# Kernel optimization log

Measured on AMD Instinct MI355X. Metric: run time of the kernel, lower is better.

## Reference

```python
import jax, jax.numpy as jnp
import numpy as np

B, N, H, HD = 2, 512, 1024, 512


def setup_inputs() -> dict:
    key = jax.random.key(0)
    ks = jax.random.split(key, 9)
    s = 0.02
    return {
        "emb": jax.random.normal(ks[0], (B, N, H), jnp.float32),
        # start detector: Linear(H->HD), ReLU, Linear(HD->1)
        "W_s1": jax.random.normal(ks[1], (H, HD), jnp.float32) * s,
        "b_s1": jax.random.normal(ks[2], (HD,), jnp.float32) * s,
        "w_s2": jax.random.normal(ks[3], (HD,), jnp.float32) * s,
        "b_s2": jax.random.normal(ks[4], (), jnp.float32) * s,
        # end detector: Linear(2H->HD), ReLU, Linear(HD->1)
        "W_e1": jax.random.normal(ks[5], (2 * H, HD), jnp.float32) * s,
        "b_e1": jax.random.normal(ks[6], (HD,), jnp.float32) * s,
        "w_e2": jax.random.normal(ks[7], (HD,), jnp.float32) * s,
        "b_e2": jax.random.normal(ks[8], (), jnp.float32) * s,
    }


def reference(emb, W_s1, b_s1, w_s2, b_s2, W_e1, b_e1, w_e2, b_e2):
    # start logits: (B, N)
    h_s = jax.nn.relu(jnp.einsum("bnh,hd->bnd", emb, W_s1) + b_s1)
    start_logits = jnp.einsum("bnd,d->bn", h_s, w_s2) + b_s2

    # end logits: math of cat([start_rep, end_rep]) @ W_e1 done as split matmuls
    # (avoids materializing the (B,N,N,2H) concat buffer)
    W1_start, W1_end = W_e1[:H], W_e1[H:]
    a = jnp.einsum("bih,hd->bid", emb, W1_start)  # (B, N, HD) start-token part
    c = jnp.einsum("bjh,hd->bjd", emb, W1_end)    # (B, N, HD) end-token part
    h_e = jax.nn.relu(a[:, :, None, :] + c[:, None, :, :] + b_e1)  # (B, N, N, HD)
    end_logits = jnp.einsum("bijd,d->bij", h_e, w_e2) + b_e2       # (B, N, N)

    return (start_logits, end_logits)
```

## Files before the change

kernel.cpp:

```cpp
#include <hip/hip_runtime.h>
#include <hip/hip_bf16.h>


typedef float f32x4 __attribute__((ext_vector_type(4)));
typedef float f32x2 __attribute__((ext_vector_type(2)));
typedef __bf16 bf16x8 __attribute__((ext_vector_type(8)));

static __device__ __forceinline__ unsigned short f2bf(float f) {
  unsigned int u = __builtin_bit_cast(unsigned int, f);
  u += 0x7FFFu + ((u >> 16) & 1u);
  return (unsigned short)(u >> 16);
}

__global__ __launch_bounds__(256) void prep(
    const float* __restrict__ emb, const float* __restrict__ W_s1,
    const float* __restrict__ W_e1, const float* __restrict__ b_s2,
    unsigned short* __restrict__ emb_bf, unsigned short* __restrict__ Wt_s,
    unsigned short* __restrict__ Wt_e, float* __restrict__ out) {
  __shared__ float tile[32][33];
  int bx = blockIdx.x, t = threadIdx.x;
  if (bx < 512) {
    int i = bx * 2048 + t * 8;
    f32x4 v0 = *(const f32x4*)&emb[i];
    f32x4 v1 = *(const f32x4*)&emb[i + 4];
    ushort4 o0, o1;
    o0.x = f2bf(v0[0]); o0.y = f2bf(v0[1]);
    o0.z = f2bf(v0[2]); o0.w = f2bf(v0[3]);
    o1.x = f2bf(v1[0]); o1.y = f2bf(v1[1]);
    o1.z = f2bf(v1[2]); o1.w = f2bf(v1[3]);
    *(ushort4*)&emb_bf[i] = o0;
    *(ushort4*)&emb_bf[i + 4] = o1;
  } else if (bx < 2048) {
    const float* in;
    unsigned short* o;
    int R, tid;
    if (bx < 1024) { tid = bx - 512;  in = W_s1; o = Wt_s; R = 1024; }
    else           { tid = bx - 1024; in = W_e1; o = Wt_e; R = 2048; }
    int r0 = (tid >> 4) * 32, c0 = (tid & 15) * 32;
    int a = t >> 3, b4 = t & 7;
    f32x4 v = *(const f32x4*)&in[(size_t)(r0 + a) * 512 + c0 + b4 * 4];
    tile[a][b4 * 4 + 0] = v[0];
    tile[a][b4 * 4 + 1] = v[1];
    tile[a][b4 * 4 + 2] = v[2];
    tile[a][b4 * 4 + 3] = v[3];
    __syncthreads();
    ushort4 o4;
    o4.x = f2bf(tile[b4 * 4 + 0][a]);
    o4.y = f2bf(tile[b4 * 4 + 1][a]);
    o4.z = f2bf(tile[b4 * 4 + 2][a]);
    o4.w = f2bf(tile[b4 * 4 + 3][a]);
    *(ushort4*)&o[(size_t)(c0 + a) * R + r0 + b4 * 4] = o4;
  } else {
    float v = b_s2[0];
    f32x4 o = {v, v, v, v};
    *(f32x4*)&out[t * 4] = o;
  }
}

__global__ __launch_bounds__(128) void gemm_fused(
    const unsigned short* __restrict__ Aemb,
    const unsigned short* __restrict__ Wt_s,
    const unsigned short* __restrict__ Wt_e,
    const float* __restrict__ b_s1, const float* __restrict__ w_s2,
    const float* __restrict__ b_e1, float* __restrict__ out,
    float* __restrict__ A_mat, unsigned short* __restrict__ C_bf) {
  __shared__ unsigned short Al[64][72];
  __shared__ unsigned short Bl[32][72];
  int z = blockIdx.z;
  int n0 = blockIdx.x * 32;
  int m0 = blockIdx.y * 64;
  const unsigned short* Bmat = (z == 0) ? Wt_s : Wt_e;
  int bstride = (z == 0) ? 1024 : 2048;
  int bofs = (z == 2) ? 1024 : 0;

  int t = threadIdx.x, lane = t & 63, wave = t >> 6;
  int wm = wave * 32;
  int lm = lane & 15, g = lane >> 4;

  f32x4 acc[2][2];
#pragma unroll
  for (int mi = 0; mi < 2; ++mi)
#pragma unroll
    for (int ni = 0; ni < 2; ++ni) acc[mi][ni] = (f32x4){0.f, 0.f, 0.f, 0.f};

  int ar = t >> 1, ah = (t & 1) * 32;
  int br = t >> 2, bs = (t & 3) * 16;
  for (int k0 = 0; k0 < 1024; k0 += 64) {
    __syncthreads();
    const unsigned short* ap = &Aemb[(size_t)(m0 + ar) * 1024 + k0 + ah];
    *(uint4*)&Al[ar][ah + 0]  = *(const uint4*)(ap + 0);
    *(uint4*)&Al[ar][ah + 8]  = *(const uint4*)(ap + 8);
    *(uint4*)&Al[ar][ah + 16] = *(const uint4*)(ap + 16);
    *(uint4*)&Al[ar][ah + 24] = *(const uint4*)(ap + 24);
    const unsigned short* bp =
        &Bmat[(size_t)(n0 + br) * bstride + bofs + k0 + bs];
    *(uint4*)&Bl[br][bs + 0] = *(const uint4*)(bp + 0);
    *(uint4*)&Bl[br][bs + 8] = *(const uint4*)(bp + 8);
    __syncthreads();
#pragma unroll
    for (int kk = 0; kk < 2; ++kk) {
      bf16x8 af[2], bf[2];
#pragma unroll
      for (int mi = 0; mi < 2; ++mi)
        af[mi] = *(const bf16x8*)&Al[wm + mi * 16 + lm][kk * 32 + g * 8];
#pragma unroll
      for (int ni = 0; ni < 2; ++ni)
        bf[ni] = *(const bf16x8*)&Bl[ni * 16 + lm][kk * 32 + g * 8];
#pragma unroll
      for (int mi = 0; mi < 2; ++mi)
#pragma unroll
        for (int ni = 0; ni < 2; ++ni)
          acc[mi][ni] = __builtin_amdgcn_mfma_f32_16x16x32_bf16(
              af[mi], bf[ni], acc[mi][ni], 0, 0, 0);
    }
  }

  int col0 = n0 + lm, col1 = n0 + 16 + lm;
  if (z == 0) {
    float bs0 = b_s1[col0], bs1 = b_s1[col1];
    float ws0 = w_s2[col0], ws1 = w_s2[col1];
#pragma unroll
    for (int mi = 0; mi < 2; ++mi)
#pragma unroll
      for (int r = 0; r < 4; ++r) {
        float s = fmaxf(acc[mi][0][r] + bs0, 0.f) * ws0 +
                  fmaxf(acc[mi][1][r] + bs1, 0.f) * ws1;
        s += __shfl_xor(s, 1);
        s += __shfl_xor(s, 2);
        s += __shfl_xor(s, 4);
        s += __shfl_xor(s, 8);
        if (lm == 0) atomicAdd(&out[m0 + wm + mi * 16 + g * 4 + r], s);
      }
  } else if (z == 1) {
#pragma unroll
    for (int mi = 0; mi < 2; ++mi)
#pragma unroll
      for (int r = 0; r < 4; ++r) {
        int row = m0 + wm + mi * 16 + g * 4 + r;
        A_mat[(size_t)row * 512 + col0] = acc[mi][0][r];
        A_mat[(size_t)row * 512 + col1] = acc[mi][1][r];
      }
  } else {
    float b0 = b_e1[col0], b1 = b_e1[col1];
#pragma unroll
    for (int mi = 0; mi < 2; ++mi)
#pragma unroll
      for (int r = 0; r < 4; ++r) {
        int row = m0 + wm + mi * 16 + g * 4 + r;
        C_bf[(size_t)row * 512 + col0] = f2bf(acc[mi][0][r] + b0);
        C_bf[(size_t)row * 512 + col1] = f2bf(acc[mi][1][r] + b1);
      }
  }
}

__global__ __launch_bounds__(512) void pairwise(
    const float* __restrict__ A_mat, const unsigned short* __restrict__ C_bf,
    const float* __restrict__ w_e2, const float* __restrict__ b_e2,
    float* __restrict__ out) {
  __shared__ f32x2 As_p[32][32];
  __shared__ unsigned int Cs_b[32][64];
  __shared__ f32x2 wl2[256];
  int t = threadIdx.x;
  int b = blockIdx.z;
  int j0 = blockIdx.x * 64, i0 = blockIdx.y * 32;

  if (t < 256) wl2[t] = *(const f32x2*)&w_e2[2 * t];
  float be2 = b_e2[0];

  int ti = t >> 5, tj = t & 31;
  f32x2 acc2[2][2];
#pragma unroll
  for (int q = 0; q < 2; ++q)
#pragma unroll
    for (int r = 0; r < 2; ++r) acc2[q][r] = (f32x2){0.f, 0.f};

  const float* Ab = A_mat + (size_t)(b * 512 + i0) * 512;
  const unsigned short* Cb = C_bf + (size_t)(b * 512 + j0) * 512;
  int si = t & 31, sq = t >> 5;
  int sj = t & 63, s2 = t >> 6;
  f32x2 z2 = {0.f, 0.f};

  for (int ch = 0; ch < 8; ++ch) {
    __syncthreads();
    {
      f32x4 va = *(const f32x4*)&Ab[(size_t)si * 512 + ch * 64 + sq * 4];
      As_p[sq * 2 + 0][si] = (f32x2){va[0], va[1]};
      As_p[sq * 2 + 1][si] = (f32x2){va[2], va[3]};
      uint4 vc = *(const uint4*)&Cb[(size_t)sj * 512 + ch * 64 + s2 * 8];
      Cs_b[s2 * 4 + 0][sj] = vc.x;
      Cs_b[s2 * 4 + 1][sj] = vc.y;
      Cs_b[s2 * 4 + 2][sj] = vc.z;
      Cs_b[s2 * 4 + 3][sj] = vc.w;
    }
    __syncthreads();
#pragma unroll 8
    for (int dp = 0; dp < 32; ++dp) {
      f32x2 w2 = wl2[ch * 32 + dp];
      f32x4 av = *(const f32x4*)&As_p[dp][ti * 2];
      uint2 cu = *(const uint2*)&Cs_b[dp][tj * 2];
      f32x2 a0 = {av[0], av[1]}, a1 = {av[2], av[3]};
      f32x2 c0 = {__builtin_bit_cast(float, cu.x << 16),
                  __builtin_bit_cast(float, cu.x & 0xFFFF0000u)};
      f32x2 c1 = {__builtin_bit_cast(float, cu.y << 16),
                  __builtin_bit_cast(float, cu.y & 0xFFFF0000u)};
      acc2[0][0] += __builtin_elementwise_max(a0 + c0, z2) * w2;
      acc2[0][1] += __builtin_elementwise_max(a0 + c1, z2) * w2;
      acc2[1][0] += __builtin_elementwise_max(a1 + c0, z2) * w2;
      acc2[1][1] += __builtin_elementwise_max(a1 + c1, z2) * w2;
    }
  }

  float* oe = out + 1024;
#pragma unroll
  for (int q = 0; q < 2; ++q) {
    int i = i0 + ti * 2 + q;
    float2 vv;
    vv.x = acc2[q][0][0] + acc2[q][0][1] + be2;
    vv.y = acc2[q][1][0] + acc2[q][1][1] + be2;
    *(float2*)&oe[(size_t)(b * 512 + i) * 512 + j0 + tj * 2] = vv;
  }
}

extern "C" void kernel_launch(void* const* d_in, const int* in_sizes, int n_in,
                              void* d_out, int out_size, void* d_ws,
                              size_t ws_size, hipStream_t stream) {
  const float* emb  = (const float*)d_in[0];
  const float* W_s1 = (const float*)d_in[1];
  const float* b_s1 = (const float*)d_in[2];
  const float* w_s2 = (const float*)d_in[3];
  const float* b_s2 = (const float*)d_in[4];
  const float* W_e1 = (const float*)d_in[5];
  const float* b_e1 = (const float*)d_in[6];
  const float* w_e2 = (const float*)d_in[7];
  const float* b_e2 = (const float*)d_in[8];
  float* out = (float*)d_out;

  char* ws = (char*)d_ws;
  unsigned short* emb_bf = (unsigned short*)(ws);
  unsigned short* Wt_s = (unsigned short*)(ws + 2u * (1u << 20));
  unsigned short* Wt_e = (unsigned short*)(ws + 3u * (1u << 20));
  float* A_mat = (float*)(ws + 5u * (1u << 20));
  unsigned short* C_bf = (unsigned short*)(ws + 7u * (1u << 20));

  hipLaunchKernelGGL(prep, dim3(2049), dim3(256), 0, stream,
                     emb, W_s1, W_e1, b_s2, emb_bf, Wt_s, Wt_e, out);
  hipLaunchKernelGGL(gemm_fused, dim3(16, 16, 3), dim3(128), 0, stream,
                     emb_bf, Wt_s, Wt_e, b_s1, w_s2, b_e1, out, A_mat, C_bf);
  hipLaunchKernelGGL(pairwise, dim3(8, 16, 2), dim3(512), 0, stream,
                     A_mat, C_bf, w_e2, b_e2, out);
}
```

Baseline: 131.9 us.

## Widen GEMM tile to 64x64 with four waves and keep C in fp32

The GEMM block tile grows from 64x32 to 64x64 with 256 threads arranged as a 2x2 wave grid, which halves the grid size and improves operand reuse from LDS. The intermediate C matrix is now stored as fp32 instead of bf16, so the pairwise kernel no longer unpacks bf16 in its inner loop but loads twice as many bytes of C from global memory and through LDS. This removes the bf16 rounding of C, which improves accuracy. The fewer blocks may lower occupancy across the GPU.

```diff
diff --git a/kernel.cpp b/kernel.cpp
--- a/kernel.cpp
+++ b/kernel.cpp
@@ -57,24 +57,24 @@
   }
 }
 
-__global__ __launch_bounds__(128) void gemm_fused(
+__global__ __launch_bounds__(256) void gemm_fused(
     const unsigned short* __restrict__ Aemb,
     const unsigned short* __restrict__ Wt_s,
     const unsigned short* __restrict__ Wt_e,
     const float* __restrict__ b_s1, const float* __restrict__ w_s2,
     const float* __restrict__ b_e1, float* __restrict__ out,
-    float* __restrict__ A_mat, unsigned short* __restrict__ C_bf) {
+    float* __restrict__ A_mat, float* __restrict__ C_mat) {
   __shared__ unsigned short Al[64][72];
-  __shared__ unsigned short Bl[32][72];
+  __shared__ unsigned short Bl[64][72];
   int z = blockIdx.z;
-  int n0 = blockIdx.x * 32;
+  int n0 = blockIdx.x * 64;
   int m0 = blockIdx.y * 64;
   const unsigned short* Bmat = (z == 0) ? Wt_s : Wt_e;
   int bstride = (z == 0) ? 1024 : 2048;
   int bofs = (z == 2) ? 1024 : 0;
 
   int t = threadIdx.x, lane = t & 63, wave = t >> 6;
-  int wm = wave * 32;
+  int wm = (wave >> 1) * 32, wn = (wave & 1) * 32;
   int lm = lane & 15, g = lane >> 4;
 
   f32x4 acc[2][2];
@@ -83,19 +83,16 @@
 #pragma unroll
     for (int ni = 0; ni < 2; ++ni) acc[mi][ni] = (f32x4){0.f, 0.f, 0.f, 0.f};
 
-  int ar = t >> 1, ah = (t & 1) * 32;
-  int br = t >> 2, bs = (t & 3) * 16;
+  int sr = t >> 2, sc = (t & 3) * 16;
   for (int k0 = 0; k0 < 1024; k0 += 64) {
     __syncthreads();
-    const unsigned short* ap = &Aemb[(size_t)(m0 + ar) * 1024 + k0 + ah];
-    *(uint4*)&Al[ar][ah + 0]  = *(const uint4*)(ap + 0);
-    *(uint4*)&Al[ar][ah + 8]  = *(const uint4*)(ap + 8);
-    *(uint4*)&Al[ar][ah + 16] = *(const uint4*)(ap + 16);
-    *(uint4*)&Al[ar][ah + 24] = *(const uint4*)(ap + 24);
+    const unsigned short* ap = &Aemb[(size_t)(m0 + sr) * 1024 + k0 + sc];
+    *(uint4*)&Al[sr][sc] = *(const uint4*)ap;
+    *(uint4*)&Al[sr][sc + 8] = *(const uint4*)(ap + 8);
     const unsigned short* bp =
-        &Bmat[(size_t)(n0 + br) * bstride + bofs + k0 + bs];
-    *(uint4*)&Bl[br][bs + 0] = *(const uint4*)(bp + 0);
-    *(uint4*)&Bl[br][bs + 8] = *(const uint4*)(bp + 8);
+        &Bmat[(size_t)(n0 + sr) * bstride + bofs + k0 + sc];
+    *(uint4*)&Bl[sr][sc] = *(const uint4*)bp;
+    *(uint4*)&Bl[sr][sc + 8] = *(const uint4*)(bp + 8);
     __syncthreads();
 #pragma unroll
     for (int kk = 0; kk < 2; ++kk) {
@@ -105,7 +102,7 @@
         af[mi] = *(const bf16x8*)&Al[wm + mi * 16 + lm][kk * 32 + g * 8];
 #pragma unroll
       for (int ni = 0; ni < 2; ++ni)
-        bf[ni] = *(const bf16x8*)&Bl[ni * 16 + lm][kk * 32 + g * 8];
+        bf[ni] = *(const bf16x8*)&Bl[wn + ni * 16 + lm][kk * 32 + g * 8];
 #pragma unroll
       for (int mi = 0; mi < 2; ++mi)
 #pragma unroll
@@ -115,7 +112,7 @@
     }
   }
 
-  int col0 = n0 + lm, col1 = n0 + 16 + lm;
+  int col0 = n0 + wn + lm, col1 = n0 + wn + 16 + lm;
   if (z == 0) {
     float bs0 = b_s1[col0], bs1 = b_s1[col1];
     float ws0 = w_s2[col0], ws1 = w_s2[col1];
@@ -147,18 +144,18 @@
 #pragma unroll
       for (int r = 0; r < 4; ++r) {
         int row = m0 + wm + mi * 16 + g * 4 + r;
-        C_bf[(size_t)row * 512 + col0] = f2bf(acc[mi][0][r] + b0);
-        C_bf[(size_t)row * 512 + col1] = f2bf(acc[mi][1][r] + b1);
+        C_mat[(size_t)row * 512 + col0] = acc[mi][0][r] + b0;
+        C_mat[(size_t)row * 512 + col1] = acc[mi][1][r] + b1;
       }
   }
 }
 
 __global__ __launch_bounds__(512) void pairwise(
-    const float* __restrict__ A_mat, const unsigned short* __restrict__ C_bf,
+    const float* __restrict__ A_mat, const float* __restrict__ C_mat,
     const float* __restrict__ w_e2, const float* __restrict__ b_e2,
     float* __restrict__ out) {
   __shared__ f32x2 As_p[32][32];
-  __shared__ unsigned int Cs_b[32][64];
+  __shared__ f32x2 Cs_p[32][64];
   __shared__ f32x2 wl2[256];
   int t = threadIdx.x;
   int b = blockIdx.z;
@@ -175,7 +172,7 @@
     for (int r = 0; r < 2; ++r) acc2[q][r] = (f32x2){0.f, 0.f};
 
   const float* Ab = A_mat + (size_t)(b * 512 + i0) * 512;
-  const unsigned short* Cb = C_bf + (size_t)(b * 512 + j0) * 512;
+  const float* Cb = C_mat + (size_t)(b * 512 + j0) * 512;
   int si = t & 31, sq = t >> 5;
   int sj = t & 63, s2 = t >> 6;
   f32x2 z2 = {0.f, 0.f};
@@ -186,23 +183,21 @@
       f32x4 va = *(const f32x4*)&Ab[(size_t)si * 512 + ch * 64 + sq * 4];
       As_p[sq * 2 + 0][si] = (f32x2){va[0], va[1]};
       As_p[sq * 2 + 1][si] = (f32x2){va[2], va[3]};
-      uint4 vc = *(const uint4*)&Cb[(size_t)sj * 512 + ch * 64 + s2 * 8];
-      Cs_b[s2 * 4 + 0][sj] = vc.x;
-      Cs_b[s2 * 4 + 1][sj] = vc.y;
-      Cs_b[s2 * 4 + 2][sj] = vc.z;
-      Cs_b[s2 * 4 + 3][sj] = vc.w;
+      f32x4 v0 = *(const f32x4*)&Cb[(size_t)sj * 512 + ch * 64 + s2 * 8];
+      f32x4 v1 = *(const f32x4*)&Cb[(size_t)sj * 512 + ch * 64 + s2 * 8 + 4];
+      Cs_p[s2 * 4 + 0][sj] = (f32x2){v0[0], v0[1]};
+      Cs_p[s2 * 4 + 1][sj] = (f32x2){v0[2], v0[3]};
+      Cs_p[s2 * 4 + 2][sj] = (f32x2){v1[0], v1[1]};
+      Cs_p[s2 * 4 + 3][sj] = (f32x2){v1[2], v1[3]};
     }
     __syncthreads();
 #pragma unroll 8
     for (int dp = 0; dp < 32; ++dp) {
       f32x2 w2 = wl2[ch * 32 + dp];
       f32x4 av = *(const f32x4*)&As_p[dp][ti * 2];
-      uint2 cu = *(const uint2*)&Cs_b[dp][tj * 2];
+      f32x4 cv = *(const f32x4*)&Cs_p[dp][tj * 2];
       f32x2 a0 = {av[0], av[1]}, a1 = {av[2], av[3]};
-      f32x2 c0 = {__builtin_bit_cast(float, cu.x << 16),
-                  __builtin_bit_cast(float, cu.x & 0xFFFF0000u)};
-      f32x2 c1 = {__builtin_bit_cast(float, cu.y << 16),
-                  __builtin_bit_cast(float, cu.y & 0xFFFF0000u)};
+      f32x2 c0 = {cv[0], cv[1]}, c1 = {cv[2], cv[3]};
       acc2[0][0] += __builtin_elementwise_max(a0 + c0, z2) * w2;
       acc2[0][1] += __builtin_elementwise_max(a0 + c1, z2) * w2;
       acc2[1][0] += __builtin_elementwise_max(a1 + c0, z2) * w2;
@@ -240,12 +235,12 @@
   unsigned short* Wt_s = (unsigned short*)(ws + 2u * (1u << 20));
   unsigned short* Wt_e = (unsigned short*)(ws + 3u * (1u << 20));
   float* A_mat = (float*)(ws + 5u * (1u << 20));
-  unsigned short* C_bf = (unsigned short*)(ws + 7u * (1u << 20));
+  float* C_mat = (float*)(ws + 7u * (1u << 20));
 
   hipLaunchKernelGGL(prep, dim3(2049), dim3(256), 0, stream,
                      emb, W_s1, W_e1, b_s2, emb_bf, Wt_s, Wt_e, out);
-  hipLaunchKernelGGL(gemm_fused, dim3(16, 16, 3), dim3(128), 0, stream,
-                     emb_bf, Wt_s, Wt_e, b_s1, w_s2, b_e1, out, A_mat, C_bf);
+  hipLaunchKernelGGL(gemm_fused, dim3(8, 16, 3), dim3(256), 0, stream,
+                     emb_bf, Wt_s, Wt_e, b_s1, w_s2, b_e1, out, A_mat, C_mat);
   hipLaunchKernelGGL(pairwise, dim3(8, 16, 2), dim3(512), 0, stream,
-                     A_mat, C_bf, w_e2, b_e2, out);
-}
+                     A_mat, C_mat, w_e2, b_e2, out);
+}
```

New measurement: 126.1 us. -4.4%, faster.
